# Kernel tuning notes

Measured on AMD Instinct MI355X. Metric: run time of the kernel, lower is better.

The kernel has to match this reference:

```python
import jax, jax.numpy as jnp
import numpy as np

S = 2048        # seq_len (number of rigid bodies)
D = 256         # node_dim
H = 16          # num_heads
C = 64          # num_channels
SPATIAL_DIM = 3
QUATERNION_DIM = 4


def setup_inputs() -> dict:
    key = jax.random.key(0)
    ks = jax.random.split(key, 9)
    nodes = jax.random.normal(ks[0], (S, D), jnp.float32)
    pos = jax.random.normal(ks[1], (S, 2 * SPATIAL_DIM), jnp.float32)
    rot = jax.random.normal(ks[2], (S, QUATERNION_DIM), jnp.float32)
    w = 0.02
    Wn = jax.random.normal(ks[3], (2 * H * C, D), jnp.float32) * w
    bn = jnp.zeros((2 * H * C,), jnp.float32)
    Wp = jax.random.normal(ks[4], (2 * H * C, 2 * SPATIAL_DIM), jnp.float32) * w
    bp = jnp.zeros((2 * H * C,), jnp.float32)
    Wr = jax.random.normal(ks[5], (2 * H * C, QUATERNION_DIM), jnp.float32) * w  # no bias
    Wv = jax.random.normal(ks[6], (3 * H * D, D), jnp.float32) * w
    bv = jnp.zeros((3 * H * D,), jnp.float32)
    return {"nodes": nodes, "pos": pos, "rot": rot,
            "Wn": Wn, "bn": bn, "Wp": Wp, "bp": bp, "Wr": Wr,
            "Wv": Wv, "bv": bv}


def _kq(x, W, b):
    # eqx.nn.Linear: y = W @ x + b, vmapped over seq -> x @ W.T + b
    y = x @ W.T
    if b is not None:
        y = y + b
    y = y.reshape(x.shape[0], H, 2 * C)
    k, q = jnp.split(y, 2, axis=-1)  # each (S, H, C)
    return k, q


def reference(nodes, pos, rot, Wn, bn, Wp, bp, Wr, Wv, bv):
    seq_len = nodes.shape[0]
    nodes_k, nodes_q = _kq(nodes, Wn, bn)
    pos_k, pos_q = _kq(pos, Wp, bp)
    rot_k, rot_q = _kq(rot, Wr, None)
    k = jnp.concatenate([nodes_k, pos_k, rot_k], axis=-2)  # (S, 3H, C)
    q = jnp.concatenate([nodes_q, pos_q, rot_q], axis=-2)  # (S, 3H, C)
    val = (nodes @ Wv.T + bv).reshape(seq_len, 3 * H, D)   # (S, 3H, D)
    logits = jnp.einsum('ihc,jhc->ijh', k, q)              # (S, S, 3H)
    # square the rotation-source logits (last H of the 3H head axis)
    logits = logits.at[..., -H:].set(jnp.square(logits[..., -H:]))
    logits = logits / jnp.sqrt(jnp.float32(H))
    att = jax.nn.softmax(logits, axis=-2)                  # softmax over key axis j
    out = jnp.einsum('ijh,jhd->id', att, val)              # (S, D)
    return out
```

## Files before the change

kernel.cpp:

```cpp
#include <hip/hip_runtime.h>
#include <hip/hip_bf16.h>

typedef __bf16 bf16;
typedef __attribute__((ext_vector_type(8)))  __bf16 bf16x8;
typedef __attribute__((ext_vector_type(4)))  __bf16 bf16x4;
typedef __attribute__((ext_vector_type(4)))  float  f32x4;

#define SEQ   2048
#define NDIM  256
#define NH3   48
#define CH    64
#define SQS   72
#define SVS   72
#define SPS   72
#define VTS   2176

#define OFF_NODES 0
#define OFF_POS   524288
#define OFF_ROT   536576
#define OFF_WN    544768
#define OFF_BN    1069056
#define OFF_WP    1071104
#define OFF_BP    1083392
#define OFF_WR    1085440
#define OFF_WV    1093632
#define OFF_BV    4239360
#define TOT_IN    4251648

__device__ bf16  g_in[TOT_IN];
__device__ bf16  g_k [NH3 * SEQ * CH];
__device__ bf16  g_q [NH3 * SEQ * CH];
__device__ bf16  g_vt[NH3 * NDIM * VTS];
__device__ float g_part[(size_t)NH3 * SEQ * NDIM];
__device__ int   g_isf32;

__global__ __launch_bounds__(256) void detect_k(const unsigned short* __restrict__ p) {
    __shared__ int cff, czero;
    if (threadIdx.x == 0) { cff = 0; czero = 0; }
    __syncthreads();
    int ff = 0, zz = 0;
    for (int r = 0; r < 64; ++r) {
        int idx = threadIdx.x * 64 + r;
        unsigned short u = p[idx];
        if (((u >> 7) & 0xFF) == 0xFF) ff++;
        if (((idx & 1) == 0) && (u == 0)) zz++;
    }
    if (ff) atomicAdd(&cff, ff);
    if (zz) atomicAdd(&czero, zz);
    __syncthreads();
    if (threadIdx.x == 0) g_isf32 = (cff > 2 || czero > 6000) ? 1 : 0;
}

__global__ __launch_bounds__(256) void convert_k(
    const void* s0, const void* s1, const void* s2, const void* s3, const void* s4,
    const void* s5, const void* s6, const void* s7, const void* s8, const void* s9)
{
    const void* srcs[10] = {s0, s1, s2, s3, s4, s5, s6, s7, s8, s9};
    const int   szs[10]  = {524288, 12288, 8192, 524288, 2048, 12288, 2048, 8192, 3145728, 12288};
    const int   offs[10] = {OFF_NODES, OFF_POS, OFF_ROT, OFF_WN, OFF_BN,
                            OFF_WP, OFF_BP, OFF_WR, OFF_WV, OFF_BV};
    const int y = blockIdx.y;
    const void* src = srcs[y];
    bf16* dst = g_in + offs[y];
    const int n = szs[y];
    const int isf = g_isf32;
    const int stride = gridDim.x * 256 * 4;
    for (int i = (blockIdx.x * 256 + threadIdx.x) * 4; i < n; i += stride) {
        bf16x4 o;
        if (isf) {
            float4 v = *(const float4*)((const float*)src + i);
            o[0] = (bf16)v.x; o[1] = (bf16)v.y; o[2] = (bf16)v.z; o[3] = (bf16)v.w;
        } else {
            o = *(const bf16x4*)((const bf16*)src + i);
        }
        *(bf16x4*)(dst + i) = o;
    }
}

__global__ __launch_bounds__(256) void proj_nodes_kq()
{
    __shared__ __align__(16) bf16 sB[64 * 264];
    const bf16* nodes = g_in + OFF_NODES;
    const bf16* Wn    = g_in + OFF_WN;
    const bf16* bn    = g_in + OFF_BN;
    const int t    = threadIdx.x;
    const int bx   = blockIdx.x;
    const int xcd  = bx & 7;
    const int rest = bx >> 3;
    const int f0   = (xcd * 4 + (rest & 3)) * 64;
    const int s0   = (rest >> 2) * 64;

    for (int rep = 0; rep < 8; ++rep) {
        int idx = t + rep * 256;
        int row = idx >> 5, chunk = idx & 31;
        *(bf16x8*)&sB[row * 264 + chunk * 8] =
            *(const bf16x8*)&Wn[(f0 + row) * 256 + chunk * 8];
    }
    __syncthreads();

    const int w = t >> 6, lane = t & 63;
    const int l15 = lane & 15, quad = lane >> 4;

    f32x4 acc[4] = {{}, {}, {}, {}};
    const bf16* arow = nodes + (s0 + w * 16 + l15) * 256 + quad * 8;
#pragma unroll
    for (int kc = 0; kc < 8; ++kc) {
        bf16x8 af = *(const bf16x8*)(arow + kc * 32);
#pragma unroll
        for (int ft = 0; ft < 4; ++ft) {
            bf16x8 bfr = *(const bf16x8*)&sB[(ft * 16 + l15) * 264 + kc * 32 + quad * 8];
            acc[ft] = __builtin_amdgcn_mfma_f32_16x16x32_bf16(af, bfr, acc[ft], 0, 0, 0);
        }
    }
#pragma unroll
    for (int ft = 0; ft < 4; ++ft) {
        int f = f0 + ft * 16 + l15;
        float bias = (float)bn[f];
        int h = f >> 7, c2 = f & 127;
        bf16* base = (c2 < 64) ? (g_k + h * SEQ * CH + c2)
                               : (g_q + h * SEQ * CH + (c2 - 64));
#pragma unroll
        for (int r = 0; r < 4; ++r) {
            int s = s0 + w * 16 + quad * 4 + r;
            base[s * CH] = (bf16)(acc[ft][r] + bias);
        }
    }
}

__global__ __launch_bounds__(256) void proj_posrot_kq()
{
    const bf16* pos  = g_in + OFF_POS;
    const bf16* rotq = g_in + OFF_ROT;
    const bf16* Wp   = g_in + OFF_WP;
    const bf16* bp   = g_in + OFF_BP;
    const bf16* Wr   = g_in + OFF_WR;
    int id = blockIdx.x * 256 + threadIdx.x;
    int fg  = id & 511;
    int s   = (id >> 9) & 2047;
    int src = id >> 20;
    int f0  = fg * 4;
    float y[4]; int h;
    if (src == 0) {
#pragma unroll
        for (int j = 0; j < 4; ++j) {
            float a = (float)bp[f0 + j];
#pragma unroll
            for (int x = 0; x < 6; ++x)
                a += (float)pos[s * 6 + x] * (float)Wp[(f0 + j) * 6 + x];
            y[j] = a;
        }
        h = 16 + (f0 >> 7);
    } else {
#pragma unroll
        for (int j = 0; j < 4; ++j) {
            float a = 0.f;
#pragma unroll
            for (int x = 0; x < 4; ++x)
                a += (float)rotq[s * 4 + x] * (float)Wr[(f0 + j) * 4 + x];
            y[j] = a;
        }
        h = 32 + (f0 >> 7);
    }
    bf16x4 o;
#pragma unroll
    for (int j = 0; j < 4; ++j) o[j] = (bf16)y[j];
    int c2 = f0 & 127;
    if (c2 < 64) *(bf16x4*)&g_k[(h * SEQ + s) * CH + c2]        = o;
    else         *(bf16x4*)&g_q[(h * SEQ + s) * CH + (c2 - 64)] = o;
}

__global__ __launch_bounds__(256) void proj_v()
{
    __shared__ __align__(16) bf16 sB[64 * 264];
    __shared__ __align__(16) bf16 sO[64 * 72];
    const bf16* nodes = g_in + OFF_NODES;
    const bf16* Wv    = g_in + OFF_WV;
    const bf16* bv    = g_in + OFF_BV;
    const int t    = threadIdx.x;
    const int bx   = blockIdx.x;
    const int xcd  = bx & 7;
    const int rest = bx >> 3;
    const int f0   = (xcd * 24 + (rest % 24)) * 64;
    const int s0   = (rest / 24) * 64;

    for (int rep = 0; rep < 8; ++rep) {
        int idx = t + rep * 256;
        int row = idx >> 5, chunk = idx & 31;
        *(bf16x8*)&sB[row * 264 + chunk * 8] =
            *(const bf16x8*)&Wv[(size_t)(f0 + row) * 256 + chunk * 8];
    }
    __syncthreads();

    const int w = t >> 6, lane = t & 63;
    const int l15 = lane & 15, quad = lane >> 4;

    f32x4 acc[4] = {{}, {}, {}, {}};
    const bf16* arow = nodes + (s0 + w * 16 + l15) * 256 + quad * 8;
#pragma unroll
    for (int kc = 0; kc < 8; ++kc) {
        bf16x8 af = *(const bf16x8*)(arow + kc * 32);
#pragma unroll
        for (int ft = 0; ft < 4; ++ft) {
            bf16x8 bfr = *(const bf16x8*)&sB[(ft * 16 + l15) * 264 + kc * 32 + quad * 8];
            acc[ft] = __builtin_amdgcn_mfma_f32_16x16x32_bf16(af, bfr, acc[ft], 0, 0, 0);
        }
    }
    __syncthreads();
#pragma unroll
    for (int ft = 0; ft < 4; ++ft) {
        int n = f0 + ft * 16 + l15;
        float bias = (float)bv[n];
#pragma unroll
        for (int r = 0; r < 4; ++r) {
            sO[(ft * 16 + l15) * 72 + (quad * 4 + r) * 4 + w] = (bf16)(acc[ft][r] + bias);
        }
    }
    __syncthreads();
    for (int rep = 0; rep < 2; ++rep) {
        int idx = t + rep * 256;
        int row = idx >> 3, chunk = idx & 7;
        *(bf16x8*)&g_vt[(size_t)(f0 + row) * VTS + s0 + chunk * 8] =
            *(const bf16x8*)&sO[row * 72 + chunk * 8];
    }
}

__global__ __launch_bounds__(512, 4) void attn_k()
{
    const int bx  = blockIdx.x;
    const int xcd = bx & 7;
    const int sub = bx >> 3;
    const int h   = xcd * 6 + (sub % 6);
    const int it  = sub / 6;
    const int i0  = it * 128;
    const int t   = threadIdx.x;
    const int w   = t >> 6, lane = t & 63;
    const int l15 = lane & 15, quad = lane >> 4;
    const bool rot = (h >= 32);

    __shared__ __align__(16) bf16 sQ[64 * SQS];
    __shared__ __align__(16) bf16 sV[256 * SVS];
    __shared__ __align__(16) bf16 sP[128 * SPS];
    __shared__ float sL[128];

    const bf16* kb = g_k  + h * SEQ * CH;
    const bf16* qb = g_q  + h * SEQ * CH;
    const bf16* vb = g_vt + (size_t)h * NDIM * VTS;

    bf16x8 kf0 = *(const bf16x8*)&kb[(i0 + w * 16 + l15) * CH + quad * 8];
    bf16x8 kf1 = *(const bf16x8*)&kb[(i0 + w * 16 + l15) * CH + 32 + quad * 8];

    const int ih = w >> 2, dq = w & 3;

    const int qrow = t >> 3, qch = t & 7;

    f32x4 acc[4][4];
#pragma unroll
    for (int a = 0; a < 4; ++a)
#pragma unroll
        for (int b = 0; b < 4; ++b) acc[a][b] = (f32x4){0.f, 0.f, 0.f, 0.f};
    f32x4 lp = {0.f, 0.f, 0.f, 0.f};

    bf16x8 qpre, vpre[4];
    qpre = *(const bf16x8*)&qb[t * 8];
#pragma unroll
    for (int rep = 0; rep < 4; ++rep) {
        int idx = t + rep * 512;
        vpre[rep] = *(const bf16x8*)&vb[(size_t)(idx >> 3) * VTS + (idx & 7) * 8];
    }
    *(bf16x8*)&sQ[qrow * SQS + qch * 8] = qpre;
#pragma unroll
    for (int rep = 0; rep < 4; ++rep) {
        int idx = t + rep * 512;
        *(bf16x8*)&sV[(idx >> 3) * SVS + (idx & 7) * 8] = vpre[rep];
    }
    __syncthreads();

    for (int st = 0; st < 32; ++st) {
        f32x4 sjb[4];
#pragma unroll
        for (int jb = 0; jb < 4; ++jb) {
            bf16x8 q0 = *(const bf16x8*)&sQ[(jb * 16 + l15) * SQS + quad * 8];
            bf16x8 q1 = *(const bf16x8*)&sQ[(jb * 16 + l15) * SQS + 32 + quad * 8];
            f32x4 sa = {};
            sa = __builtin_amdgcn_mfma_f32_16x16x32_bf16(kf0, q0, sa, 0, 0, 0);
            sa = __builtin_amdgcn_mfma_f32_16x16x32_bf16(kf1, q1, sa, 0, 0, 0);
            sjb[jb] = sa;
        }

#pragma unroll
        for (int r = 0; r < 4; ++r) {
            bf16x4 pk;
#pragma unroll
            for (int jb = 0; jb < 4; ++jb) {
                float d = sjb[jb][r];
                float x = rot ? (d * d * 0.25f) : (d * 0.25f);
                x = fminf(x, 60.f);
                float p = __expf(x);
                lp[r] += p;
                pk[jb] = (bf16)p;
            }
            *(bf16x4*)&sP[(w * 16 + quad * 4 + r) * SPS + l15 * 4] = pk;
        }
        __syncthreads();

        if (st < 31) {
            const bf16* qn = qb + (st + 1) * 4096;
            const bf16* vn = vb + (st + 1) * 64;
            qpre = *(const bf16x8*)&qn[t * 8];
#pragma unroll
            for (int rep = 0; rep < 4; ++rep) {
                int idx = t + rep * 512;
                vpre[rep] = *(const bf16x8*)&vn[(size_t)(idx >> 3) * VTS + (idx & 7) * 8];
            }
        }

#pragma unroll
        for (int kc = 0; kc < 2; ++kc) {
            bf16x8 ap[4], vf[4];
#pragma unroll
            for (int itr = 0; itr < 4; ++itr)
                ap[itr] = *(const bf16x8*)&sP[(ih * 64 + itr * 16 + l15) * SPS + kc * 32 + quad * 8];
#pragma unroll
            for (int dt = 0; dt < 4; ++dt)
                vf[dt] = *(const bf16x8*)&sV[(dq * 64 + dt * 16 + l15) * SVS + kc * 32 + quad * 8];
#pragma unroll
            for (int itr = 0; itr < 4; ++itr)
#pragma unroll
                for (int dt = 0; dt < 4; ++dt)
                    acc[itr][dt] = __builtin_amdgcn_mfma_f32_16x16x32_bf16(
                        ap[itr], vf[dt], acc[itr][dt], 0, 0, 0);
        }
        __syncthreads();

        if (st < 31) {
            *(bf16x8*)&sQ[qrow * SQS + qch * 8] = qpre;
#pragma unroll
            for (int rep = 0; rep < 4; ++rep) {
                int idx = t + rep * 512;
                *(bf16x8*)&sV[(idx >> 3) * SVS + (idx & 7) * 8] = vpre[rep];
            }
            __syncthreads();
        }
    }

#pragma unroll
    for (int off = 1; off < 16; off <<= 1) {
#pragma unroll
        for (int r = 0; r < 4; ++r) lp[r] += __shfl_xor(lp[r], off, 64);
    }
    if (l15 == 0) *(f32x4*)&sL[w * 16 + quad * 4] = lp;
    __syncthreads();

    float* pb = g_part + (size_t)h * SEQ * NDIM;
#pragma unroll
    for (int itr = 0; itr < 4; ++itr) {
        f32x4 lv = *(const f32x4*)&sL[ih * 64 + itr * 16 + quad * 4];
#pragma unroll
        for (int r = 0; r < 4; ++r) {
            float inv = 1.0f / lv[r];
            float* ob = &pb[(size_t)(i0 + ih * 64 + itr * 16 + quad * 4 + r) * NDIM + dq * 64 + l15];
#pragma unroll
            for (int dt = 0; dt < 4; ++dt)
                ob[dt * 16] = acc[itr][dt][r] * inv;
        }
    }
}

__global__ __launch_bounds__(256) void finalize_k(float* __restrict__ out) {
    int idx = (blockIdx.x * 256 + threadIdx.x) * 4;
    f32x4 s = {0.f, 0.f, 0.f, 0.f};
#pragma unroll
    for (int hh = 0; hh < NH3; ++hh)
        s += *(const f32x4*)&g_part[(size_t)hh * SEQ * NDIM + idx];
    *(f32x4*)&out[idx] = s;
}

extern "C" void kernel_launch(void* const* d_in, const int* in_sizes, int n_in,
                              void* d_out, int out_size, void* d_ws, size_t ws_size,
                              hipStream_t stream) {
    detect_k <<<dim3(1),        dim3(256), 0, stream>>>((const unsigned short*)d_in[8]);
    convert_k<<<dim3(768, 10),  dim3(256), 0, stream>>>(d_in[0], d_in[1], d_in[2], d_in[3],
                                                        d_in[4], d_in[5], d_in[6], d_in[7],
                                                        d_in[8], d_in[9]);
    proj_nodes_kq <<<dim3(1024),  dim3(256), 0, stream>>>();
    proj_posrot_kq<<<dim3(8192),  dim3(256), 0, stream>>>();
    proj_v        <<<dim3(6144),  dim3(256), 0, stream>>>();
    attn_k        <<<dim3(768),   dim3(512), 0, stream>>>();
    finalize_k    <<<dim3(512),   dim3(256), 0, stream>>>((float*)d_out);
}
```

Before: 333.7 us.

## Merge projection kernels and retile attention QK so warps split key columns

The three projection kernels (nodes K/Q, pos/rot K/Q, V) are merged into one launch that picks its role from the block index, which removes two launch gaps and lets the small pos/rot work overlap the GEMM blocks. In the attention kernel, each warp now computes a 32-row by 32-column score tile instead of 16 rows by 64 columns. Each warp therefore holds four K fragments and reads half as many Q fragments from shared memory. Row sums are now partial per column half and are combined through shared memory (reusing sQ) before normalisation, at the cost of more registers and narrower 2-element stores into sP.

```diff
diff --git a/kernel.cpp b/kernel.cpp
--- a/kernel.cpp
+++ b/kernel.cpp
@@ -4,6 +4,7 @@
 typedef __bf16 bf16;
 typedef __attribute__((ext_vector_type(8)))  __bf16 bf16x8;
 typedef __attribute__((ext_vector_type(4)))  __bf16 bf16x4;
+typedef __attribute__((ext_vector_type(2)))  __bf16 bf16x2;
 typedef __attribute__((ext_vector_type(4)))  float  f32x4;
 
 #define SEQ   2048
@@ -77,64 +78,94 @@
     }
 }
 
-__global__ __launch_bounds__(256) void proj_nodes_kq()
+__global__ __launch_bounds__(256) void proj_all()
 {
     __shared__ __align__(16) bf16 sB[64 * 264];
-    const bf16* nodes = g_in + OFF_NODES;
-    const bf16* Wn    = g_in + OFF_WN;
-    const bf16* bn    = g_in + OFF_BN;
-    const int t    = threadIdx.x;
-    const int bx   = blockIdx.x;
-    const int xcd  = bx & 7;
-    const int rest = bx >> 3;
-    const int f0   = (xcd * 4 + (rest & 3)) * 64;
-    const int s0   = (rest >> 2) * 64;
-
-    for (int rep = 0; rep < 8; ++rep) {
-        int idx = t + rep * 256;
-        int row = idx >> 5, chunk = idx & 31;
-        *(bf16x8*)&sB[row * 264 + chunk * 8] =
-            *(const bf16x8*)&Wn[(f0 + row) * 256 + chunk * 8];
-    }
-    __syncthreads();
-
-    const int w = t >> 6, lane = t & 63;
-    const int l15 = lane & 15, quad = lane >> 4;
-
-    f32x4 acc[4] = {{}, {}, {}, {}};
-    const bf16* arow = nodes + (s0 + w * 16 + l15) * 256 + quad * 8;
-#pragma unroll
-    for (int kc = 0; kc < 8; ++kc) {
-        bf16x8 af = *(const bf16x8*)(arow + kc * 32);
-#pragma unroll
-        for (int ft = 0; ft < 4; ++ft) {
-            bf16x8 bfr = *(const bf16x8*)&sB[(ft * 16 + l15) * 264 + kc * 32 + quad * 8];
-            acc[ft] = __builtin_amdgcn_mfma_f32_16x16x32_bf16(af, bfr, acc[ft], 0, 0, 0);
-        }
-    }
-#pragma unroll
-    for (int ft = 0; ft < 4; ++ft) {
-        int f = f0 + ft * 16 + l15;
-        float bias = (float)bn[f];
-        int h = f >> 7, c2 = f & 127;
-        bf16* base = (c2 < 64) ? (g_k + h * SEQ * CH + c2)
-                               : (g_q + h * SEQ * CH + (c2 - 64));
-#pragma unroll
-        for (int r = 0; r < 4; ++r) {
-            int s = s0 + w * 16 + quad * 4 + r;
-            base[s * CH] = (bf16)(acc[ft][r] + bias);
-        }
-    }
-}
-
-__global__ __launch_bounds__(256) void proj_posrot_kq()
-{
+    __shared__ __align__(16) bf16 sO[64 * 72];
+    const int t  = threadIdx.x;
+    const int bx = blockIdx.x;
+
+    if (bx < 7168) {
+        const bool isV = (bx >= 1024);
+        const bf16* nodes = g_in + OFF_NODES;
+        const bf16* W     = g_in + (isV ? OFF_WV : OFF_WN);
+        const bf16* bias  = g_in + (isV ? OFF_BV : OFF_BN);
+        int f0, s0;
+        if (!isV) {
+            const int xcd = bx & 7, rest = bx >> 3;
+            f0 = (xcd * 4 + (rest & 3)) * 64;
+            s0 = (rest >> 2) * 64;
+        } else {
+            const int b2 = bx - 1024;
+            const int xcd = b2 & 7, rest = b2 >> 3;
+            f0 = (xcd * 24 + (rest % 24)) * 64;
+            s0 = (rest / 24) * 64;
+        }
+
+        for (int rep = 0; rep < 8; ++rep) {
+            int idx = t + rep * 256;
+            int row = idx >> 5, chunk = idx & 31;
+            *(bf16x8*)&sB[row * 264 + chunk * 8] =
+                *(const bf16x8*)&W[(size_t)(f0 + row) * 256 + chunk * 8];
+        }
+        __syncthreads();
+
+        const int w = t >> 6, lane = t & 63;
+        const int l15 = lane & 15, quad = lane >> 4;
+
+        f32x4 acc[4] = {{}, {}, {}, {}};
+        const bf16* arow = nodes + (s0 + w * 16 + l15) * 256 + quad * 8;
+#pragma unroll
+        for (int kc = 0; kc < 8; ++kc) {
+            bf16x8 af = *(const bf16x8*)(arow + kc * 32);
+#pragma unroll
+            for (int ft = 0; ft < 4; ++ft) {
+                bf16x8 bfr = *(const bf16x8*)&sB[(ft * 16 + l15) * 264 + kc * 32 + quad * 8];
+                acc[ft] = __builtin_amdgcn_mfma_f32_16x16x32_bf16(af, bfr, acc[ft], 0, 0, 0);
+            }
+        }
+        if (!isV) {
+#pragma unroll
+            for (int ft = 0; ft < 4; ++ft) {
+                int f = f0 + ft * 16 + l15;
+                float b = (float)bias[f];
+                int h = f >> 7, c2 = f & 127;
+                bf16* base = (c2 < 64) ? (g_k + h * SEQ * CH + c2)
+                                       : (g_q + h * SEQ * CH + (c2 - 64));
+#pragma unroll
+                for (int r = 0; r < 4; ++r) {
+                    int s = s0 + w * 16 + quad * 4 + r;
+                    base[s * CH] = (bf16)(acc[ft][r] + b);
+                }
+            }
+        } else {
+            __syncthreads();
+#pragma unroll
+            for (int ft = 0; ft < 4; ++ft) {
+                int n = f0 + ft * 16 + l15;
+                float b = (float)bias[n];
+#pragma unroll
+                for (int r = 0; r < 4; ++r) {
+                    sO[(ft * 16 + l15) * 72 + (quad * 4 + r) * 4 + w] = (bf16)(acc[ft][r] + b);
+                }
+            }
+            __syncthreads();
+            for (int rep = 0; rep < 2; ++rep) {
+                int idx = t + rep * 256;
+                int row = idx >> 3, chunk = idx & 7;
+                *(bf16x8*)&g_vt[(size_t)(f0 + row) * VTS + s0 + chunk * 8] =
+                    *(const bf16x8*)&sO[row * 72 + chunk * 8];
+            }
+        }
+        return;
+    }
+
     const bf16* pos  = g_in + OFF_POS;
     const bf16* rotq = g_in + OFF_ROT;
     const bf16* Wp   = g_in + OFF_WP;
     const bf16* bp   = g_in + OFF_BP;
     const bf16* Wr   = g_in + OFF_WR;
-    int id = blockIdx.x * 256 + threadIdx.x;
+    int id = (bx - 7168) * 256 + t;
     int fg  = id & 511;
     int s   = (id >> 9) & 2047;
     int src = id >> 20;
@@ -167,61 +198,6 @@
     int c2 = f0 & 127;
     if (c2 < 64) *(bf16x4*)&g_k[(h * SEQ + s) * CH + c2]        = o;
     else         *(bf16x4*)&g_q[(h * SEQ + s) * CH + (c2 - 64)] = o;
-}
-
-__global__ __launch_bounds__(256) void proj_v()
-{
-    __shared__ __align__(16) bf16 sB[64 * 264];
-    __shared__ __align__(16) bf16 sO[64 * 72];
-    const bf16* nodes = g_in + OFF_NODES;
-    const bf16* Wv    = g_in + OFF_WV;
-    const bf16* bv    = g_in + OFF_BV;
-    const int t    = threadIdx.x;
-    const int bx   = blockIdx.x;
-    const int xcd  = bx & 7;
-    const int rest = bx >> 3;
-    const int f0   = (xcd * 24 + (rest % 24)) * 64;
-    const int s0   = (rest / 24) * 64;
-
-    for (int rep = 0; rep < 8; ++rep) {
-        int idx = t + rep * 256;
-        int row = idx >> 5, chunk = idx & 31;
-        *(bf16x8*)&sB[row * 264 + chunk * 8] =
-            *(const bf16x8*)&Wv[(size_t)(f0 + row) * 256 + chunk * 8];
-    }
-    __syncthreads();
-
-    const int w = t >> 6, lane = t & 63;
-    const int l15 = lane & 15, quad = lane >> 4;
-
-    f32x4 acc[4] = {{}, {}, {}, {}};
-    const bf16* arow = nodes + (s0 + w * 16 + l15) * 256 + quad * 8;
-#pragma unroll
-    for (int kc = 0; kc < 8; ++kc) {
-        bf16x8 af = *(const bf16x8*)(arow + kc * 32);
-#pragma unroll
-        for (int ft = 0; ft < 4; ++ft) {
-            bf16x8 bfr = *(const bf16x8*)&sB[(ft * 16 + l15) * 264 + kc * 32 + quad * 8];
-            acc[ft] = __builtin_amdgcn_mfma_f32_16x16x32_bf16(af, bfr, acc[ft], 0, 0, 0);
-        }
-    }
-    __syncthreads();
-#pragma unroll
-    for (int ft = 0; ft < 4; ++ft) {
-        int n = f0 + ft * 16 + l15;
-        float bias = (float)bv[n];
-#pragma unroll
-        for (int r = 0; r < 4; ++r) {
-            sO[(ft * 16 + l15) * 72 + (quad * 4 + r) * 4 + w] = (bf16)(acc[ft][r] + bias);
-        }
-    }
-    __syncthreads();
-    for (int rep = 0; rep < 2; ++rep) {
-        int idx = t + rep * 256;
-        int row = idx >> 3, chunk = idx & 7;
-        *(bf16x8*)&g_vt[(size_t)(f0 + row) * VTS + s0 + chunk * 8] =
-            *(const bf16x8*)&sO[row * 72 + chunk * 8];
-    }
 }
 
 __global__ __launch_bounds__(512, 4) void attn_k()
@@ -240,14 +216,19 @@
     __shared__ __align__(16) bf16 sQ[64 * SQS];
     __shared__ __align__(16) bf16 sV[256 * SVS];
     __shared__ __align__(16) bf16 sP[128 * SPS];
-    __shared__ float sL[128];
 
     const bf16* kb = g_k  + h * SEQ * CH;
     const bf16* qb = g_q  + h * SEQ * CH;
     const bf16* vb = g_vt + (size_t)h * NDIM * VTS;
 
-    bf16x8 kf0 = *(const bf16x8*)&kb[(i0 + w * 16 + l15) * CH + quad * 8];
-    bf16x8 kf1 = *(const bf16x8*)&kb[(i0 + w * 16 + l15) * CH + 32 + quad * 8];
+    const int ia = w >> 1, jh = w & 1;
+    bf16x8 kfr[2][2];
+#pragma unroll
+    for (int itk = 0; itk < 2; ++itk)
+#pragma unroll
+        for (int kc = 0; kc < 2; ++kc)
+            kfr[itk][kc] = *(const bf16x8*)&kb[(i0 + ia * 32 + itk * 16 + l15) * CH
+                                               + kc * 32 + quad * 8];
 
     const int ih = w >> 2, dq = w & 3;
 
@@ -258,7 +239,9 @@
     for (int a = 0; a < 4; ++a)
 #pragma unroll
         for (int b = 0; b < 4; ++b) acc[a][b] = (f32x4){0.f, 0.f, 0.f, 0.f};
-    f32x4 lp = {0.f, 0.f, 0.f, 0.f};
+    float lp8[8];
+#pragma unroll
+    for (int r = 0; r < 8; ++r) lp8[r] = 0.f;
 
     bf16x8 qpre, vpre[4];
     qpre = *(const bf16x8*)&qb[t * 8];
@@ -276,31 +259,37 @@
     __syncthreads();
 
     for (int st = 0; st < 32; ++st) {
-        f32x4 sjb[4];
-#pragma unroll
-        for (int jb = 0; jb < 4; ++jb) {
-            bf16x8 q0 = *(const bf16x8*)&sQ[(jb * 16 + l15) * SQS + quad * 8];
-            bf16x8 q1 = *(const bf16x8*)&sQ[(jb * 16 + l15) * SQS + 32 + quad * 8];
-            f32x4 sa = {};
-            sa = __builtin_amdgcn_mfma_f32_16x16x32_bf16(kf0, q0, sa, 0, 0, 0);
-            sa = __builtin_amdgcn_mfma_f32_16x16x32_bf16(kf1, q1, sa, 0, 0, 0);
-            sjb[jb] = sa;
-        }
-
-#pragma unroll
-        for (int r = 0; r < 4; ++r) {
-            bf16x4 pk;
-#pragma unroll
-            for (int jb = 0; jb < 4; ++jb) {
-                float d = sjb[jb][r];
-                float x = rot ? (d * d * 0.25f) : (d * 0.25f);
-                x = fminf(x, 60.f);
-                float p = __expf(x);
-                lp[r] += p;
-                pk[jb] = (bf16)p;
-            }
-            *(bf16x4*)&sP[(w * 16 + quad * 4 + r) * SPS + l15 * 4] = pk;
-        }
+        f32x4 sjb[2][2];
+#pragma unroll
+        for (int jt = 0; jt < 2; ++jt) {
+            bf16x8 q0 = *(const bf16x8*)&sQ[(jh * 32 + jt * 16 + l15) * SQS + quad * 8];
+            bf16x8 q1 = *(const bf16x8*)&sQ[(jh * 32 + jt * 16 + l15) * SQS + 32 + quad * 8];
+#pragma unroll
+            for (int itk = 0; itk < 2; ++itk) {
+                f32x4 sa = {};
+                sa = __builtin_amdgcn_mfma_f32_16x16x32_bf16(kfr[itk][0], q0, sa, 0, 0, 0);
+                sa = __builtin_amdgcn_mfma_f32_16x16x32_bf16(kfr[itk][1], q1, sa, 0, 0, 0);
+                sjb[itk][jt] = sa;
+            }
+        }
+
+#pragma unroll
+        for (int itk = 0; itk < 2; ++itk)
+#pragma unroll
+            for (int r = 0; r < 4; ++r) {
+                bf16x2 pk;
+#pragma unroll
+                for (int jt = 0; jt < 2; ++jt) {
+                    float d = sjb[itk][jt][r];
+                    float x = rot ? (d * d * 0.25f) : (d * 0.25f);
+                    x = fminf(x, 60.f);
+                    float p = __expf(x);
+                    lp8[itk * 4 + r] += p;
+                    pk[jt] = (bf16)p;
+                }
+                *(bf16x2*)&sP[(ia * 32 + itk * 16 + quad * 4 + r) * SPS
+                              + l15 * 4 + jh * 2] = pk;
+            }
         __syncthreads();
 
         if (st < 31) {
@@ -343,21 +332,29 @@
         }
     }
 
+    float* sLp = (float*)sQ;
 #pragma unroll
     for (int off = 1; off < 16; off <<= 1) {
 #pragma unroll
-        for (int r = 0; r < 4; ++r) lp[r] += __shfl_xor(lp[r], off, 64);
-    }
-    if (l15 == 0) *(f32x4*)&sL[w * 16 + quad * 4] = lp;
+        for (int r = 0; r < 8; ++r) lp8[r] += __shfl_xor(lp8[r], off, 64);
+    }
+    if (l15 == 0) {
+#pragma unroll
+        for (int itk = 0; itk < 2; ++itk) {
+            f32x4 v = {lp8[itk * 4 + 0], lp8[itk * 4 + 1], lp8[itk * 4 + 2], lp8[itk * 4 + 3]};
+            *(f32x4*)&sLp[jh * 128 + ia * 32 + itk * 16 + quad * 4] = v;
+        }
+    }
     __syncthreads();
 
     float* pb = g_part + (size_t)h * SEQ * NDIM;
 #pragma unroll
     for (int itr = 0; itr < 4; ++itr) {
-        f32x4 lv = *(const f32x4*)&sL[ih * 64 + itr * 16 + quad * 4];
+        f32x4 lv0 = *(const f32x4*)&sLp[ih * 64 + itr * 16 + quad * 4];
+        f32x4 lv1 = *(const f32x4*)&sLp[128 + ih * 64 + itr * 16 + quad * 4];
 #pragma unroll
         for (int r = 0; r < 4; ++r) {
-            float inv = 1.0f / lv[r];
+            float inv = 1.0f / (lv0[r] + lv1[r]);
             float* ob = &pb[(size_t)(i0 + ih * 64 + itr * 16 + quad * 4 + r) * NDIM + dq * 64 + l15];
 #pragma unroll
             for (int dt = 0; dt < 4; ++dt)
@@ -382,9 +379,7 @@
     convert_k<<<dim3(768, 10),  dim3(256), 0, stream>>>(d_in[0], d_in[1], d_in[2], d_in[3],
                                                         d_in[4], d_in[5], d_in[6], d_in[7],
                                                         d_in[8], d_in[9]);
-    proj_nodes_kq <<<dim3(1024),  dim3(256), 0, stream>>>();
-    proj_posrot_kq<<<dim3(8192),  dim3(256), 0, stream>>>();
-    proj_v        <<<dim3(6144),  dim3(256), 0, stream>>>();
-    attn_k        <<<dim3(768),   dim3(512), 0, stream>>>();
-    finalize_k    <<<dim3(512),   dim3(256), 0, stream>>>((float*)d_out);
-}
+    proj_all  <<<dim3(15360),   dim3(256), 0, stream>>>();
+    attn_k    <<<dim3(768),     dim3(512), 0, stream>>>();
+    finalize_k<<<dim3(512),     dim3(256), 0, stream>>>((float*)d_out);
+}
```

Measured after the change: 392.2 us. 17.5% more time.
